# Kernel optimization log

Hardware: AMD Instinct MI355X
Metric: run time of the kernel (lower is better)

Reference implementation:

```python
import jax, jax.numpy as jnp
import numpy as np

B, D, F, P = 65536, 256, 512, 256


def setup_inputs() -> dict:
    key = jax.random.key(0)
    k_x, k_f, k_p, k_a, k_b, k_t = jax.random.split(key, 6)
    x = jax.random.normal(k_x, (B, D), dtype=jnp.float32)
    # reset_parameters: uniform(-0.27, 1)
    features = jax.random.uniform(k_f, (F, D), dtype=jnp.float32, minval=-0.27, maxval=1.0)
    prototypes = jax.random.uniform(k_p, (P, D), dtype=jnp.float32, minval=-0.27, maxval=1.0)
    # alpha/beta/theta init to zeros in the module; use small random values so the
    # output is non-trivial for kernel correctness checking.
    alpha = jax.random.normal(k_a, (1,), dtype=jnp.float32) * 0.1
    beta = jax.random.normal(k_b, (1,), dtype=jnp.float32) * 0.1
    theta = jax.random.normal(k_t, (1,), dtype=jnp.float32) * 0.1
    return {"x": x, "features": features, "prototypes": prototypes,
            "alpha": alpha, "beta": beta, "theta": theta}


def reference(x, features, prototypes, alpha, beta, theta):
    # Shared projections
    x_features = x @ features.T                 # [B, F]
    p_features = prototypes @ features.T        # [P, F]
    x_present = jax.nn.relu(x_features)         # [B, F]
    p_present = jax.nn.relu(p_features)         # [P, F]
    x_weighted = x_features * x_present         # [B, F]
    p_weighted = p_features * p_present         # [P, F]

    # Tversky terms
    common = x_weighted @ p_weighted.T                          # [B, P]
    x_weighted_sum = jnp.sum(x_weighted, axis=1, keepdims=True)  # [B, 1]
    x_p_interaction = x_weighted @ p_present.T                  # [B, P]
    x_distinctive = x_weighted_sum - x_p_interaction            # [B, P]
    p_weighted_sum = jnp.sum(p_weighted, axis=1)[None, :]        # [1, P]
    x_p_weighted_interaction = x_present @ p_weighted.T         # [B, P]
    p_distinctive = p_weighted_sum - x_p_weighted_interaction   # [B, P]

    return theta * common - alpha * x_distinctive - beta * p_distinctive
```

## Files before the change

kernel.cpp:

```cpp
#include <hip/hip_runtime.h>
#include <cstdint>
#include <cstddef>

#define Bsz 65536
#define Dsz 256
#define Fsz 512
#define Psz 256

typedef __attribute__((ext_vector_type(8))) short short8;
typedef __attribute__((ext_vector_type(4))) short short4v;
typedef __attribute__((ext_vector_type(4))) float float4v;
typedef __attribute__((ext_vector_type(16))) float float16v;

__device__ inline short f2bf(float f) {
    unsigned u = __builtin_bit_cast(unsigned, f);
    u = (u + 0x7FFFu + ((u >> 16) & 1u)) >> 16;
    return (short)u;
}
__device__ inline float bf2f(short s) {
    unsigned u = ((unsigned)(unsigned short)s) << 16;
    return __builtin_bit_cast(float, u);
}


__global__ void k_prep(const float* __restrict__ features, short* __restrict__ featbB,
                       float* __restrict__ pws_neg) {
    int idx = blockIdx.x * 256 + threadIdx.x;
    int f = idx >> 5, d0 = (idx & 31) * 8;
    float4v v0 = *(const float4v*)(features + (size_t)f * Dsz + d0);
    float4v v1 = *(const float4v*)(features + (size_t)f * Dsz + d0 + 4);
    short8 s;
    s[0] = f2bf(v0.x); s[1] = f2bf(v0.y); s[2] = f2bf(v0.z); s[3] = f2bf(v0.w);
    s[4] = f2bf(v1.x); s[5] = f2bf(v1.y); s[6] = f2bf(v1.z); s[7] = f2bf(v1.w);
    int lane = (f & 15) + 16 * ((d0 >> 3) & 3);
    size_t o = (size_t)(f >> 4) * 4096 + (size_t)(d0 >> 5) * 512 + (size_t)lane * 8;
    *(short8*)&featbB[o] = s;
    if (idx < Psz) pws_neg[idx] = 0.f;
}

#define SBPITCH 136

__global__ __launch_bounds__(256, 2) void k_pside(
    const float* __restrict__ prototypes, const short* __restrict__ featbB,
    const float* __restrict__ beta_p,
    short* __restrict__ pwB, short* __restrict__ pmB, float* __restrict__ pws_neg)
{
    __shared__ char lds[35840];
    short* As = (short*)lds;
    short* Sb = (short*)lds;

    const int t = threadIdx.x;
    const int w = t >> 6, lane = t & 63, l15 = lane & 15, l4 = lane >> 4;
    const int rowg = blockIdx.x >> 2, nc = blockIdx.x & 3;
    const float beta = *beta_p;

    float4v acc[4][4];
    #pragma unroll
    for (int a = 0; a < 4; ++a)
        #pragma unroll
        for (int b = 0; b < 4; ++b) acc[a][b] = (float4v){0.f, 0.f, 0.f, 0.f};

    const float* pbase = prototypes + (size_t)rowg * 128 * Dsz;

    for (int kc = 0; kc < 4; ++kc) {
        __syncthreads();
        #pragma unroll
        for (int j = 0; j < 8; ++j) {
            int idx = j * 1024 + t * 4;
            int r = idx >> 6, c = idx & 63;
            float4v v = *(const float4v*)(pbase + (size_t)r * Dsz + kc * 64 + c);
            int unit = r * 8 + ((c >> 3) ^ (r & 7));
            short4v s; s.x = f2bf(v.x); s.y = f2bf(v.y); s.z = f2bf(v.z); s.w = f2bf(v.w);
            *(short4v*)((char*)As + unit * 16 + (c & 7) * 2) = s;
        }
        __syncthreads();
        #pragma unroll
        for (int kk = 0; kk < 2; ++kk) {
            short8 af[4], bf[4];
            const int k8 = kk * 4 + l4;
            #pragma unroll
            for (int tm = 0; tm < 4; ++tm) {
                int m = (w & 1) * 64 + tm * 16 + l15;
                af[tm] = *(const short8*)&As[(m * 8 + (k8 ^ (m & 7))) * 8];
            }
            #pragma unroll
            for (int tn = 0; tn < 4; ++tn) {
                int fcb = nc * 8 + (w >> 1) * 4 + tn;
                bf[tn] = *(const short8*)&featbB[(size_t)fcb * 4096 +
                                                 (size_t)(kc * 2 + kk) * 512 + (size_t)lane * 8];
            }
            #pragma unroll
            for (int tm = 0; tm < 4; ++tm)
                #pragma unroll
                for (int tn = 0; tn < 4; ++tn)
                    acc[tm][tn] = __builtin_amdgcn_mfma_f32_16x16x32_bf16(af[tm], bf[tn], acc[tm][tn], 0, 0, 0);
        }
    }
    __syncthreads();
    #pragma unroll
    for (int tm = 0; tm < 4; ++tm)
        #pragma unroll
        for (int tn = 0; tn < 4; ++tn)
            #pragma unroll
            for (int r = 0; r < 4; ++r) {
                int row = (w & 1) * 64 + tm * 16 + l4 * 4 + r;
                int col = (w >> 1) * 64 + tn * 16 + l15;
                Sb[row * SBPITCH + col] = f2bf(acc[tm][tn][r]);
            }
    __syncthreads();
    #pragma unroll
    for (int rep = 0; rep < 8; ++rep) {
        int u = rep * 256 + t;
        int row = u >> 4, i = u & 15;
        short8 sv = *(const short8*)&Sb[row * SBPITCH + i * 8];
        short8 pwv, pmv;
        float sum = 0.f;
        #pragma unroll
        for (int e = 0; e < 8; ++e) {
            float pf = bf2f(sv[e]);
            float pp = fmaxf(pf, 0.f);
            float pw = pf * pp;
            pwv[e] = f2bf(pw);
            pmv[e] = f2bf(pp - 1.0f);
            sum += pw;
        }
        int p = rowg * 128 + row;
        int gcol = nc * 128 + i * 8;
        size_t fo = (size_t)(gcol >> 4) * 4096 + (size_t)(p >> 5) * 512 +
                    (size_t)((p & 31) + 32 * ((gcol >> 3) & 1)) * 8;
        *(short8*)&pwB[fo] = pwv;
        *(short8*)&pmB[fo] = pmv;
        #pragma unroll
        for (int mk = 1; mk < 16; mk <<= 1) sum += __shfl_xor(sum, mk, 64);
        if ((lane & 15) == 0) atomicAdd(&pws_neg[p], -beta * sum);
    }
}

__global__ __launch_bounds__(256, 2) void k_main(
    const float* __restrict__ x, const short* __restrict__ featbB,
    const short* __restrict__ pwB, const short* __restrict__ pmB,
    const float* __restrict__ pws_neg,
    const float* __restrict__ alpha_p, const float* __restrict__ beta_p,
    const float* __restrict__ theta_p, float* __restrict__ out)
{
    __shared__ short A12[4096];

    const int t = threadIdx.x;
    const int w = t >> 6, lane = t & 63, l15 = lane & 15, l4 = lane >> 4;
    const int l31 = lane & 31, half = lane >> 5;
    const float alpha = *alpha_p, beta = *beta_p, theta = *theta_p;
    const size_t row0 = (size_t)blockIdx.x * 64;

    short8 xreg[8];
    {
        const float* xr = x + (row0 + 16 * w + l15) * Dsz + l4 * 8;
        #pragma unroll
        for (int kk = 0; kk < 8; ++kk) {
            float4v v0 = *(const float4v*)(xr + kk * 32);
            float4v v1 = *(const float4v*)(xr + kk * 32 + 4);
            short8 s;
            s[0] = f2bf(v0.x); s[1] = f2bf(v0.y); s[2] = f2bf(v0.z); s[3] = f2bf(v0.w);
            s[4] = f2bf(v1.x); s[5] = f2bf(v1.y); s[6] = f2bf(v1.z); s[7] = f2bf(v1.w);
            xreg[kk] = s;
        }
    }

    float16v acc[2][2];
    #pragma unroll
    for (int a = 0; a < 2; ++a)
        #pragma unroll
        for (int b = 0; b < 2; ++b)
            #pragma unroll
            for (int e = 0; e < 16; ++e) acc[a][b][e] = 0.f;

    const int mbase = 16 * w + l4 * 4;
    const size_t lane8 = (size_t)lane * 8;
    const size_t pwoff = (size_t)w * 1024 + lane8;

    short8 fbR[2][8];
    short8 pR[2][4];

    #pragma unroll
    for (int kk = 0; kk < 8; ++kk)
        fbR[0][kk] = *(const short8*)(featbB + kk * 512 + lane8);
    pR[0][0] = *(const short8*)(pwB + pwoff);
    pR[0][1] = *(const short8*)(pwB + pwoff + 512);
    pR[0][2] = *(const short8*)(pmB + pwoff);
    pR[0][3] = *(const short8*)(pmB + pwoff + 512);

    auto body = [&](int fc, int cur, int nxt) {
        const int buf = (fc & 1) << 11;
        const int fcn = (fc + 1) & 31;

        const short* fbsrc = featbB + (size_t)fcn * 4096 + lane8;
        #pragma unroll
        for (int kk = 0; kk < 8; ++kk)
            fbR[nxt][kk] = *(const short8*)(fbsrc + kk * 512);
        pR[nxt][0] = *(const short8*)(pwB + (size_t)fcn * 4096 + pwoff);
        pR[nxt][1] = *(const short8*)(pwB + (size_t)fcn * 4096 + pwoff + 512);
        pR[nxt][2] = *(const short8*)(pmB + (size_t)fcn * 4096 + pwoff);
        pR[nxt][3] = *(const short8*)(pmB + (size_t)fcn * 4096 + pwoff + 512);

        float4v s0 = (float4v){0.f, 0.f, 0.f, 0.f};
        float4v s1 = (float4v){0.f, 0.f, 0.f, 0.f};
        #pragma unroll
        for (int kk = 0; kk < 8; kk += 2) {
            s0 = __builtin_amdgcn_mfma_f32_16x16x32_bf16(xreg[kk],     fbR[cur][kk],     s0, 0, 0, 0);
            s1 = __builtin_amdgcn_mfma_f32_16x16x32_bf16(xreg[kk + 1], fbR[cur][kk + 1], s1, 0, 0, 0);
        }

        #pragma unroll
        for (int r = 0; r < 4; ++r) {
            float sv = s0[r] + s1[r];
            float xp = fmaxf(sv, 0.f);
            float xw = sv * xp;
            int m = mbase + r;
            int swz = (m >> 2) & 3;
            A12[buf + (m * 4 + ((l15 >> 3) ^ swz)) * 8 + (l15 & 7)]       = f2bf(theta * xw + beta * xp);
            A12[buf + (m * 4 + ((2 | (l15 >> 3)) ^ swz)) * 8 + (l15 & 7)] = f2bf(alpha * xw);
        }
        __syncthreads();

        #pragma unroll
        for (int mi = 0; mi < 2; ++mi) {
            int m = 32 * mi + l31;
            int swz = (m >> 2) & 3;
            short8 a1 = *(const short8*)&A12[buf + (m * 4 + (half ^ swz)) * 8];
            short8 a2 = *(const short8*)&A12[buf + (m * 4 + ((2 | half) ^ swz)) * 8];
            acc[mi][0] = __builtin_amdgcn_mfma_f32_32x32x16_bf16(a1, pR[cur][0], acc[mi][0], 0, 0, 0);
            acc[mi][0] = __builtin_amdgcn_mfma_f32_32x32x16_bf16(a2, pR[cur][2], acc[mi][0], 0, 0, 0);
            acc[mi][1] = __builtin_amdgcn_mfma_f32_32x32x16_bf16(a1, pR[cur][1], acc[mi][1], 0, 0, 0);
            acc[mi][1] = __builtin_amdgcn_mfma_f32_32x32x16_bf16(a2, pR[cur][3], acc[mi][1], 0, 0, 0);
        }
    };

    #pragma unroll 1
    for (int fc = 0; fc < 32; fc += 2) {
        body(fc,     0, 1);
        body(fc + 1, 1, 0);
    }

    #pragma unroll
    for (int ni = 0; ni < 2; ++ni) {
        int col = 64 * w + 32 * ni + l31;
        float pn_ = pws_neg[col];
        #pragma unroll
        for (int mi = 0; mi < 2; ++mi)
            #pragma unroll
            for (int rg = 0; rg < 16; ++rg) {
                size_t grow = row0 + 32 * mi + (rg & 3) + 8 * (rg >> 2) + 4 * half;
                out[grow * Psz + col] = acc[mi][ni][rg] + pn_;
            }
    }
}

extern "C" void kernel_launch(void* const* d_in, const int* in_sizes, int n_in,
                              void* d_out, int out_size, void* d_ws, size_t ws_size,
                              hipStream_t stream) {
    const float* x          = (const float*)d_in[0];
    const float* features   = (const float*)d_in[1];
    const float* prototypes = (const float*)d_in[2];
    const float* alpha      = (const float*)d_in[3];
    const float* beta       = (const float*)d_in[4];
    const float* theta      = (const float*)d_in[5];
    float* out = (float*)d_out;

    char* ws = (char*)d_ws;
    short* featbB  = (short*)(ws);
    short* pwB     = (short*)(ws + 262144);
    short* pmB     = (short*)(ws + 524288);
    float* pws_neg = (float*)(ws + 786432);

    hipLaunchKernelGGL(k_prep,  dim3(64),   dim3(256), 0, stream, features, featbB, pws_neg);
    hipLaunchKernelGGL(k_pside, dim3(8),    dim3(256), 0, stream, prototypes, featbB, beta,
                       pwB, pmB, pws_neg);
    hipLaunchKernelGGL(k_main,  dim3(1024), dim3(256), 0, stream, x, featbB, pwB, pmB,
                       pws_neg, alpha, beta, theta, out);
}
```

Baseline: 193.3 us.

## Fold Tversky coefficients into prototype operand and restructure main GEMM pipeline

Merges the prep and prototype kernels into one, which converts features to bf16 in LDS and writes per-slice partial sums instead of using atomics. Alpha, beta and theta are folded into a single interleaved prototype operand, so the main kernel's second GEMM takes (xw, xp) pairs with no per-element scaling. The main kernel now stages x in LDS, computes 32x32 projection tiles against register-held feature fragments, and feeds the relu products directly from accumulators into the second MFMA without an LDS round trip or barrier. The intent is to cut launches, LDS traffic and synchronization; in exchange it uses heavier register pressure and a new data layout.

Result: no change. 195.8 us (+1.3%).

```diff
diff --git a/kernel.cpp b/kernel.cpp
--- a/kernel.cpp
+++ b/kernel.cpp
@@ -11,6 +11,7 @@
 typedef __attribute__((ext_vector_type(4))) short short4v;
 typedef __attribute__((ext_vector_type(4))) float float4v;
 typedef __attribute__((ext_vector_type(16))) float float16v;
+typedef __attribute__((ext_vector_type(4))) unsigned uint4v;
 
 __device__ inline short f2bf(float f) {
     unsigned u = __builtin_bit_cast(unsigned, f);
@@ -21,236 +22,244 @@
     unsigned u = ((unsigned)(unsigned short)s) << 16;
     return __builtin_bit_cast(float, u);
 }
-
-
-__global__ void k_prep(const float* __restrict__ features, short* __restrict__ featbB,
-                       float* __restrict__ pws_neg) {
-    int idx = blockIdx.x * 256 + threadIdx.x;
-    int f = idx >> 5, d0 = (idx & 31) * 8;
-    float4v v0 = *(const float4v*)(features + (size_t)f * Dsz + d0);
-    float4v v1 = *(const float4v*)(features + (size_t)f * Dsz + d0 + 4);
-    short8 s;
-    s[0] = f2bf(v0.x); s[1] = f2bf(v0.y); s[2] = f2bf(v0.z); s[3] = f2bf(v0.w);
-    s[4] = f2bf(v1.x); s[5] = f2bf(v1.y); s[6] = f2bf(v1.z); s[7] = f2bf(v1.w);
-    int lane = (f & 15) + 16 * ((d0 >> 3) & 3);
-    size_t o = (size_t)(f >> 4) * 4096 + (size_t)(d0 >> 5) * 512 + (size_t)lane * 8;
-    *(short8*)&featbB[o] = s;
-    if (idx < Psz) pws_neg[idx] = 0.f;
-}
+__device__ inline unsigned cvt_pk_bf16(float lo, float hi) {
+    unsigned r;
+    asm("v_cvt_pk_bf16_f32 %0, %1, %2" : "=v"(r) : "v"(lo), "v"(hi));
+    return r;
+}
+
 
 #define SBPITCH 136
 
-__global__ __launch_bounds__(256, 2) void k_pside(
-    const float* __restrict__ prototypes, const short* __restrict__ featbB,
-    const float* __restrict__ beta_p,
-    short* __restrict__ pwB, short* __restrict__ pmB, float* __restrict__ pws_neg)
+__global__ __launch_bounds__(256, 2) void k_pre(
+    const float* __restrict__ prototypes, const float* __restrict__ features,
+    const float* __restrict__ alpha_p, const float* __restrict__ beta_p,
+    const float* __restrict__ theta_p,
+    short* __restrict__ featbB, short* __restrict__ pab, float* __restrict__ pws_part)
 {
-    __shared__ char lds[35840];
-    short* As = (short*)lds;
-    short* Sb = (short*)lds;
+    __shared__ char lds[65536 + 17408];
+    short* FB = (short*)lds;
+    short* As = (short*)(lds + 65536);
+    short* Sb = (short*)(lds + 65536);
 
     const int t = threadIdx.x;
     const int w = t >> 6, lane = t & 63, l15 = lane & 15, l4 = lane >> 4;
     const int rowg = blockIdx.x >> 2, nc = blockIdx.x & 3;
-    const float beta = *beta_p;
-
-    float4v acc[4][4];
-    #pragma unroll
-    for (int a = 0; a < 4; ++a)
+    const float alpha = *alpha_p, beta = *beta_p, theta = *theta_p;
+
+    #pragma unroll
+    for (int it = 0; it < 16; ++it) {
+        int u = it * 256 + t;
+        int ftl = u >> 10, dtl = (u >> 6) & 15, ln = u & 63;
+        const float* src = features + (size_t)(nc * 128 + ftl * 32 + (ln & 31)) * Dsz
+                         + dtl * 16 + (ln >> 5) * 8;
+        float4v v0 = *(const float4v*)src;
+        float4v v1 = *(const float4v*)(src + 4);
+        uint4v uv;
+        uv.x = cvt_pk_bf16(v0.x, v0.y);
+        uv.y = cvt_pk_bf16(v0.z, v0.w);
+        uv.z = cvt_pk_bf16(v1.x, v1.y);
+        uv.w = cvt_pk_bf16(v1.z, v1.w);
+        short8 sv = __builtin_bit_cast(short8, uv);
+        *(short8*)&FB[u * 8] = sv;
+        if (rowg == 0) {
+            int go = (((nc * 4 + ftl) * 16 + dtl) * 64 + ln) * 8;
+            *(short8*)&featbB[go] = sv;
+        }
+    }
+
+    float4v acc[2][4];
+    #pragma unroll
+    for (int a = 0; a < 2; ++a)
         #pragma unroll
         for (int b = 0; b < 4; ++b) acc[a][b] = (float4v){0.f, 0.f, 0.f, 0.f};
 
-    const float* pbase = prototypes + (size_t)rowg * 128 * Dsz;
+    const float* pbase = prototypes + (size_t)rowg * 64 * Dsz;
 
     for (int kc = 0; kc < 4; ++kc) {
         __syncthreads();
         #pragma unroll
-        for (int j = 0; j < 8; ++j) {
+        for (int j = 0; j < 4; ++j) {
             int idx = j * 1024 + t * 4;
             int r = idx >> 6, c = idx & 63;
             float4v v = *(const float4v*)(pbase + (size_t)r * Dsz + kc * 64 + c);
             int unit = r * 8 + ((c >> 3) ^ (r & 7));
-            short4v s; s.x = f2bf(v.x); s.y = f2bf(v.y); s.z = f2bf(v.z); s.w = f2bf(v.w);
-            *(short4v*)((char*)As + unit * 16 + (c & 7) * 2) = s;
+            short4v s4; s4.x = f2bf(v.x); s4.y = f2bf(v.y); s4.z = f2bf(v.z); s4.w = f2bf(v.w);
+            *(short4v*)((char*)As + unit * 16 + (c & 7) * 2) = s4;
         }
         __syncthreads();
         #pragma unroll
         for (int kk = 0; kk < 2; ++kk) {
-            short8 af[4], bf[4];
+            short8 af[2], bfr[4];
             const int k8 = kk * 4 + l4;
             #pragma unroll
-            for (int tm = 0; tm < 4; ++tm) {
-                int m = (w & 1) * 64 + tm * 16 + l15;
+            for (int tm = 0; tm < 2; ++tm) {
+                int m = (w & 1) * 32 + tm * 16 + l15;
                 af[tm] = *(const short8*)&As[(m * 8 + (k8 ^ (m & 7))) * 8];
             }
             #pragma unroll
             for (int tn = 0; tn < 4; ++tn) {
-                int fcb = nc * 8 + (w >> 1) * 4 + tn;
-                bf[tn] = *(const short8*)&featbB[(size_t)fcb * 4096 +
-                                                 (size_t)(kc * 2 + kk) * 512 + (size_t)lane * 8];
-            }
-            #pragma unroll
-            for (int tm = 0; tm < 4; ++tm)
+                int fl = ((w >> 1) * 4 + tn) * 16 + l15;
+                int dtl = kc * 4 + kk * 2 + (l4 >> 1);
+                int lnp = (fl & 31) + 32 * (l4 & 1);
+                bfr[tn] = *(const short8*)&FB[(((fl >> 5) * 16 + dtl) * 64 + lnp) * 8];
+            }
+            #pragma unroll
+            for (int tm = 0; tm < 2; ++tm)
                 #pragma unroll
                 for (int tn = 0; tn < 4; ++tn)
-                    acc[tm][tn] = __builtin_amdgcn_mfma_f32_16x16x32_bf16(af[tm], bf[tn], acc[tm][tn], 0, 0, 0);
+                    acc[tm][tn] = __builtin_amdgcn_mfma_f32_16x16x32_bf16(af[tm], bfr[tn], acc[tm][tn], 0, 0, 0);
         }
     }
     __syncthreads();
     #pragma unroll
-    for (int tm = 0; tm < 4; ++tm)
+    for (int tm = 0; tm < 2; ++tm)
         #pragma unroll
         for (int tn = 0; tn < 4; ++tn)
             #pragma unroll
             for (int r = 0; r < 4; ++r) {
-                int row = (w & 1) * 64 + tm * 16 + l4 * 4 + r;
+                int row = (w & 1) * 32 + tm * 16 + l4 * 4 + r;
                 int col = (w >> 1) * 64 + tn * 16 + l15;
                 Sb[row * SBPITCH + col] = f2bf(acc[tm][tn][r]);
             }
     __syncthreads();
     #pragma unroll
-    for (int rep = 0; rep < 8; ++rep) {
+    for (int rep = 0; rep < 4; ++rep) {
         int u = rep * 256 + t;
         int row = u >> 4, i = u & 15;
         short8 sv = *(const short8*)&Sb[row * SBPITCH + i * 8];
-        short8 pwv, pmv;
+        uint4v u0, u1;
         float sum = 0.f;
         #pragma unroll
         for (int e = 0; e < 8; ++e) {
             float pf = bf2f(sv[e]);
             float pp = fmaxf(pf, 0.f);
             float pw = pf * pp;
-            pwv[e] = f2bf(pw);
-            pmv[e] = f2bf(pp - 1.0f);
+            float a0 = theta * pw + alpha * (pp - 1.f);
+            float b0 = beta * pw;
             sum += pw;
-        }
-        int p = rowg * 128 + row;
-        int gcol = nc * 128 + i * 8;
-        size_t fo = (size_t)(gcol >> 4) * 4096 + (size_t)(p >> 5) * 512 +
-                    (size_t)((p & 31) + 32 * ((gcol >> 3) & 1)) * 8;
-        *(short8*)&pwB[fo] = pwv;
-        *(short8*)&pmB[fo] = pmv;
+            unsigned pk = cvt_pk_bf16(a0, b0);
+            if (e < 4) u0[e] = pk; else u1[e - 4] = pk;
+        }
+        int p = rowg * 64 + row;
+        int c = 4 * nc + (i >> 2), s2 = i & 3, pt = p >> 5;
+        int base = ((c * 4 + s2) * 8 + pt) * 512;
+        *(short8*)&pab[base + (p & 31) * 8] = __builtin_bit_cast(short8, u0);
+        *(short8*)&pab[base + ((p & 31) + 32) * 8] = __builtin_bit_cast(short8, u1);
         #pragma unroll
         for (int mk = 1; mk < 16; mk <<= 1) sum += __shfl_xor(sum, mk, 64);
-        if ((lane & 15) == 0) atomicAdd(&pws_neg[p], -beta * sum);
+        if (l15 == 0) pws_part[nc * 256 + p] = -beta * sum;
     }
 }
 
 __global__ __launch_bounds__(256, 2) void k_main(
     const float* __restrict__ x, const short* __restrict__ featbB,
-    const short* __restrict__ pwB, const short* __restrict__ pmB,
-    const float* __restrict__ pws_neg,
-    const float* __restrict__ alpha_p, const float* __restrict__ beta_p,
-    const float* __restrict__ theta_p, float* __restrict__ out)
+    const short* __restrict__ pab, const float* __restrict__ pws_part,
+    float* __restrict__ out)
 {
-    __shared__ short A12[4096];
+    __shared__ short XL[16384];
 
     const int t = threadIdx.x;
-    const int w = t >> 6, lane = t & 63, l15 = lane & 15, l4 = lane >> 4;
-    const int l31 = lane & 31, half = lane >> 5;
-    const float alpha = *alpha_p, beta = *beta_p, theta = *theta_p;
+    const int w = t >> 6, lane = t & 63, l31 = lane & 31, h = lane >> 5;
     const size_t row0 = (size_t)blockIdx.x * 64;
 
-    short8 xreg[8];
-    {
-        const float* xr = x + (row0 + 16 * w + l15) * Dsz + l4 * 8;
-        #pragma unroll
-        for (int kk = 0; kk < 8; ++kk) {
-            float4v v0 = *(const float4v*)(xr + kk * 32);
-            float4v v1 = *(const float4v*)(xr + kk * 32 + 4);
-            short8 s;
-            s[0] = f2bf(v0.x); s[1] = f2bf(v0.y); s[2] = f2bf(v0.z); s[3] = f2bf(v0.w);
-            s[4] = f2bf(v1.x); s[5] = f2bf(v1.y); s[6] = f2bf(v1.z); s[7] = f2bf(v1.w);
-            xreg[kk] = s;
-        }
-    }
-
-    float16v acc[2][2];
-    #pragma unroll
-    for (int a = 0; a < 2; ++a)
-        #pragma unroll
-        for (int b = 0; b < 2; ++b)
-            #pragma unroll
-            for (int e = 0; e < 16; ++e) acc[a][b][e] = 0.f;
-
-    const int mbase = 16 * w + l4 * 4;
-    const size_t lane8 = (size_t)lane * 8;
-    const size_t pwoff = (size_t)w * 1024 + lane8;
-
-    short8 fbR[2][8];
-    short8 pR[2][4];
-
-    #pragma unroll
-    for (int kk = 0; kk < 8; ++kk)
-        fbR[0][kk] = *(const short8*)(featbB + kk * 512 + lane8);
-    pR[0][0] = *(const short8*)(pwB + pwoff);
-    pR[0][1] = *(const short8*)(pwB + pwoff + 512);
-    pR[0][2] = *(const short8*)(pmB + pwoff);
-    pR[0][3] = *(const short8*)(pmB + pwoff + 512);
-
-    auto body = [&](int fc, int cur, int nxt) {
-        const int buf = (fc & 1) << 11;
-        const int fcn = (fc + 1) & 31;
-
-        const short* fbsrc = featbB + (size_t)fcn * 4096 + lane8;
-        #pragma unroll
-        for (int kk = 0; kk < 8; ++kk)
-            fbR[nxt][kk] = *(const short8*)(fbsrc + kk * 512);
-        pR[nxt][0] = *(const short8*)(pwB + (size_t)fcn * 4096 + pwoff);
-        pR[nxt][1] = *(const short8*)(pwB + (size_t)fcn * 4096 + pwoff + 512);
-        pR[nxt][2] = *(const short8*)(pmB + (size_t)fcn * 4096 + pwoff);
-        pR[nxt][3] = *(const short8*)(pmB + (size_t)fcn * 4096 + pwoff + 512);
-
-        float4v s0 = (float4v){0.f, 0.f, 0.f, 0.f};
-        float4v s1 = (float4v){0.f, 0.f, 0.f, 0.f};
-        #pragma unroll
-        for (int kk = 0; kk < 8; kk += 2) {
-            s0 = __builtin_amdgcn_mfma_f32_16x16x32_bf16(xreg[kk],     fbR[cur][kk],     s0, 0, 0, 0);
-            s1 = __builtin_amdgcn_mfma_f32_16x16x32_bf16(xreg[kk + 1], fbR[cur][kk + 1], s1, 0, 0, 0);
-        }
-
-        #pragma unroll
-        for (int r = 0; r < 4; ++r) {
-            float sv = s0[r] + s1[r];
-            float xp = fmaxf(sv, 0.f);
-            float xw = sv * xp;
-            int m = mbase + r;
-            int swz = (m >> 2) & 3;
-            A12[buf + (m * 4 + ((l15 >> 3) ^ swz)) * 8 + (l15 & 7)]       = f2bf(theta * xw + beta * xp);
-            A12[buf + (m * 4 + ((2 | (l15 >> 3)) ^ swz)) * 8 + (l15 & 7)] = f2bf(alpha * xw);
-        }
-        __syncthreads();
-
-        #pragma unroll
-        for (int mi = 0; mi < 2; ++mi) {
-            int m = 32 * mi + l31;
-            int swz = (m >> 2) & 3;
-            short8 a1 = *(const short8*)&A12[buf + (m * 4 + (half ^ swz)) * 8];
-            short8 a2 = *(const short8*)&A12[buf + (m * 4 + ((2 | half) ^ swz)) * 8];
-            acc[mi][0] = __builtin_amdgcn_mfma_f32_32x32x16_bf16(a1, pR[cur][0], acc[mi][0], 0, 0, 0);
-            acc[mi][0] = __builtin_amdgcn_mfma_f32_32x32x16_bf16(a2, pR[cur][2], acc[mi][0], 0, 0, 0);
-            acc[mi][1] = __builtin_amdgcn_mfma_f32_32x32x16_bf16(a1, pR[cur][1], acc[mi][1], 0, 0, 0);
-            acc[mi][1] = __builtin_amdgcn_mfma_f32_32x32x16_bf16(a2, pR[cur][3], acc[mi][1], 0, 0, 0);
-        }
-    };
+    #pragma unroll
+    for (int it = 0; it < 8; ++it) {
+        int idx = it * 256 + t;
+        int mt_i = idx >> 10, dt_i = (idx >> 6) & 15, ln = idx & 63;
+        const float* src = x + (row0 + mt_i * 32 + (ln & 31)) * Dsz + dt_i * 16 + (ln >> 5) * 8;
+        float4v v0 = *(const float4v*)src;
+        float4v v1 = *(const float4v*)(src + 4);
+        uint4v uv;
+        uv.x = cvt_pk_bf16(v0.x, v0.y);
+        uv.y = cvt_pk_bf16(v0.z, v0.w);
+        uv.z = cvt_pk_bf16(v1.x, v1.y);
+        uv.w = cvt_pk_bf16(v1.z, v1.w);
+        *(short8*)&XL[idx * 8] = __builtin_bit_cast(short8, uv);
+    }
+    __syncthreads();
+
+    const int mt = w & 1, pth = w >> 1;
+    int xoff = mt * 8192 + lane * 8;
+    const int a1off = lane * 8;
+    const int pboff = (pth * 4) * 512 + lane * 8;
+
+    float16v acc[4];
+    #pragma unroll
+    for (int a = 0; a < 4; ++a)
+        #pragma unroll
+        for (int e = 0; e < 16; ++e) acc[a][e] = 0.f;
+
+    short8 A1[16];
+    short8 PB[16];
+    #pragma unroll
+    for (int dt = 0; dt < 16; ++dt)
+        A1[dt] = *(const short8*)(featbB + a1off + dt * 512);
+    #pragma unroll
+    for (int ptl = 0; ptl < 4; ++ptl)
+        #pragma unroll
+        for (int s = 0; s < 4; ++s)
+            PB[ptl * 4 + s] = *(const short8*)(pab + pboff + s * 4096 + ptl * 512);
 
     #pragma unroll 1
-    for (int fc = 0; fc < 32; fc += 2) {
-        body(fc,     0, 1);
-        body(fc + 1, 1, 0);
-    }
-
-    #pragma unroll
-    for (int ni = 0; ni < 2; ++ni) {
-        int col = 64 * w + 32 * ni + l31;
-        float pn_ = pws_neg[col];
-        #pragma unroll
-        for (int mi = 0; mi < 2; ++mi)
-            #pragma unroll
-            for (int rg = 0; rg < 16; ++rg) {
-                size_t grow = row0 + 32 * mi + (rg & 3) + 8 * (rg >> 2) + 4 * half;
-                out[grow * Psz + col] = acc[mi][ni][rg] + pn_;
-            }
+    for (int c = 0; c < 16; ++c) {
+        asm volatile("" : "+v"(xoff));
+
+        float16v C1;
+        #pragma unroll
+        for (int e = 0; e < 16; ++e) C1[e] = 0.f;
+        #pragma unroll
+        for (int dt = 0; dt < 16; ++dt) {
+            short8 xfr = *(const short8*)&XL[xoff + dt * 512];
+            C1 = __builtin_amdgcn_mfma_f32_32x32x16_bf16(A1[dt], xfr, C1, 0, 0, 0);
+        }
+
+        {
+            const short* a1n = featbB + ((c + 1) & 15) * 8192 + a1off;
+            #pragma unroll
+            for (int dt = 0; dt < 16; ++dt)
+                A1[dt] = *(const short8*)(a1n + dt * 512);
+        }
+
+        short8 A2f[4];
+        #pragma unroll
+        for (int s = 0; s < 4; ++s) {
+            uint4v uf;
+            #pragma unroll
+            for (int q = 0; q < 4; ++q) {
+                float xf = C1[4 * s + q];
+                float xp = fmaxf(xf, 0.f);
+                float xw = xf * xp;
+                uf[q] = cvt_pk_bf16(xw, xp);
+            }
+            A2f[s] = __builtin_bit_cast(short8, uf);
+        }
+
+        #pragma unroll
+        for (int s = 0; s < 4; ++s)
+            #pragma unroll
+            for (int ptl = 0; ptl < 4; ++ptl)
+                acc[ptl] = __builtin_amdgcn_mfma_f32_32x32x16_bf16(A2f[s], PB[ptl * 4 + s], acc[ptl], 0, 0, 0);
+
+        {
+            const short* pbn = pab + ((c + 1) & 15) * 16384 + pboff;
+            #pragma unroll
+            for (int ptl = 0; ptl < 4; ++ptl)
+                #pragma unroll
+                for (int s = 0; s < 4; ++s)
+                    PB[ptl * 4 + s] = *(const short8*)(pbn + s * 4096 + ptl * 512);
+        }
+    }
+
+    #pragma unroll
+    for (int ptl = 0; ptl < 4; ++ptl) {
+        int pcol = (pth * 4 + ptl) * 32 + l31;
+        float pn = pws_part[pcol] + pws_part[256 + pcol] + pws_part[512 + pcol] + pws_part[768 + pcol];
+        #pragma unroll
+        for (int r = 0; r < 16; ++r) {
+            size_t m = row0 + mt * 32 + (r & 3) + 8 * (r >> 2) + 4 * h;
+            out[m * Psz + pcol] = acc[ptl][r] + pn;
+        }
     }
 }
 
@@ -266,14 +275,12 @@
     float* out = (float*)d_out;
 
     char* ws = (char*)d_ws;
-    short* featbB  = (short*)(ws);
-    short* pwB     = (short*)(ws + 262144);
-    short* pmB     = (short*)(ws + 524288);
-    float* pws_neg = (float*)(ws + 786432);
-
-    hipLaunchKernelGGL(k_prep,  dim3(64),   dim3(256), 0, stream, features, featbB, pws_neg);
-    hipLaunchKernelGGL(k_pside, dim3(8),    dim3(256), 0, stream, prototypes, featbB, beta,
-                       pwB, pmB, pws_neg);
-    hipLaunchKernelGGL(k_main,  dim3(1024), dim3(256), 0, stream, x, featbB, pwB, pmB,
-                       pws_neg, alpha, beta, theta, out);
-}
+    short* featbB   = (short*)(ws);
+    short* pab      = (short*)(ws + 262144);
+    float* pws_part = (float*)(ws + 786432);
+
+    hipLaunchKernelGGL(k_pre,  dim3(16),   dim3(256), 0, stream,
+                       prototypes, features, alpha, beta, theta, featbB, pab, pws_part);
+    hipLaunchKernelGGL(k_main, dim3(1024), dim3(256), 0, stream,
+                       x, featbB, pab, pws_part, out);
+}
```
